# Performance work log

Measured on AMD Instinct MI355X. Metric: run time of the kernel, lower is better.

The kernel has to match this reference:

```python
import jax, jax.numpy as jnp
import numpy as np

M_CACHE, N_MODEL, D_HEAD = 8192, 4096, 128
H_HEADS = N_MODEL // D_HEAD  # 32
SEQ_LEN = 16


def setup_inputs() -> dict:
    key = jax.random.key(0)
    ks = jax.random.split(key, 6)
    X = jax.random.normal(ks[0], (SEQ_LEN, N_MODEL), dtype=jnp.float32)
    W_q = jax.random.normal(ks[1], (N_MODEL, N_MODEL), dtype=jnp.float32) * 0.02
    W_k = jax.random.normal(ks[2], (N_MODEL, N_MODEL), dtype=jnp.float32) * 0.02
    W_v = jax.random.normal(ks[3], (N_MODEL, N_MODEL), dtype=jnp.float32) * 0.02
    cache_K = jax.random.normal(ks[4], (H_HEADS, M_CACHE, D_HEAD), dtype=jnp.float32)
    cache_V = jax.random.normal(ks[5], (H_HEADS, M_CACHE, D_HEAD), dtype=jnp.float32)
    return {"X": X, "W_q": W_q, "W_k": W_k, "W_v": W_v,
            "cache_K": cache_K, "cache_V": cache_V, "P": 4096}


def reference(X, W_q, W_k, W_v, cache_K, cache_V, P):
    S = X.shape[0]
    H, M, D = cache_K.shape
    # QKV projections, split into heads: [S, N] -> [H, S, D]
    q = (X @ W_q).reshape(S, H, D).transpose(1, 0, 2)
    k = (X @ W_k).reshape(S, H, D).transpose(1, 0, 2)
    v = (X @ W_v).reshape(S, H, D).transpose(1, 0, 2)
    # KV-cache slice write at position P
    cK = cache_K.at[:, P:P + S, :].set(k)
    cV = cache_V.at[:, P:P + S, :].set(v)
    # Unscaled attention over the FULL cache length (faithful to original)
    scores = jnp.einsum('hsd,hmd->hsm', q, cK)          # [H, S, M]
    weights = jax.nn.softmax(scores, axis=-1)
    out = jnp.einsum('hsm,hmd->hsd', weights, cV)        # [H, S, D]
    # Original does .view(S, H*D) on the [H, S, D] tensor (no transpose)
    return out.reshape(S, H * D)
```

## Files before the change

kernel.cpp:

```cpp
#include <hip/hip_runtime.h>

#define S_LEN 16
#define NMODEL 4096
#define DHEAD 128
#define HHEADS 32
#define MCACHE 8192
#define SPLITK 32
#define KSLICE (NMODEL / SPLITK)
#define CHUNK_W 32
#define NCHT (MCACHE / CHUNK_W)
#define MPAD 36

#define PART_ELEMS   ((size_t)3 * SPLITK * S_LEN * NMODEL)
#define OPART_USH    ((size_t)HHEADS * NCHT * S_LEN * DHEAD)
#define OPART_FLOATS (OPART_USH / 2)
#define REGION_ELEMS (PART_ELEMS > OPART_FLOATS ? PART_ELEMS : OPART_FLOATS)
#define STAT_ELEMS   ((size_t)HHEADS * NCHT * S_LEN)

typedef _Float16 half8 __attribute__((ext_vector_type(8)));
typedef float    f32x4 __attribute__((ext_vector_type(4)));

__device__ __forceinline__ half8 cvt8(float4 a, float4 b) {
    half8 h;
    h[0] = (_Float16)a.x; h[1] = (_Float16)a.y; h[2] = (_Float16)a.z; h[3] = (_Float16)a.w;
    h[4] = (_Float16)b.x; h[5] = (_Float16)b.y; h[6] = (_Float16)b.z; h[7] = (_Float16)b.w;
    return h;
}
__device__ __forceinline__ unsigned short f2h(float f) {
    _Float16 h = (_Float16)f; unsigned short u; __builtin_memcpy(&u, &h, 2); return u;
}
__device__ __forceinline__ float h2f(unsigned short u) {
    _Float16 h; __builtin_memcpy(&h, &u, 2); return (float)h;
}

__global__ __launch_bounds__(256) void qkv_gemm(const float* __restrict__ X,
                                                const float* __restrict__ Wq,
                                                const float* __restrict__ Wk,
                                                const float* __restrict__ Wv,
                                                float* __restrict__ part) {
    const int tid   = threadIdx.x;
    const int col2  = blockIdx.x * 256 + tid;
    const int split = blockIdx.y;
    const int mat   = blockIdx.z;
    const float* __restrict__ W = (mat == 0) ? Wq : (mat == 1) ? Wk : Wv;
    const int k0 = split * KSLICE;

    __shared__ float Xs[KSLICE][S_LEN];
    for (int i = tid; i < KSLICE * S_LEN; i += 256) {
        const int s = i & 15, k = i >> 4;
        Xs[k][s] = X[s * NMODEL + k0 + k];
    }
    __syncthreads();

    float2 acc[S_LEN];
#pragma unroll
    for (int s = 0; s < S_LEN; ++s) { acc[s].x = 0.f; acc[s].y = 0.f; }

    const float2* __restrict__ Wp = (const float2*)(W + (size_t)k0 * NMODEL) + col2;

#pragma unroll 8
    for (int k = 0; k < KSLICE; ++k) {
        const float2 w = Wp[(size_t)k * (NMODEL / 2)];
        const float4* __restrict__ xr = (const float4*)&Xs[k][0];
#pragma unroll
        for (int s4 = 0; s4 < 4; ++s4) {
            const float4 xv = xr[s4];
            acc[s4 * 4 + 0].x += xv.x * w.x;  acc[s4 * 4 + 0].y += xv.x * w.y;
            acc[s4 * 4 + 1].x += xv.y * w.x;  acc[s4 * 4 + 1].y += xv.y * w.y;
            acc[s4 * 4 + 2].x += xv.z * w.x;  acc[s4 * 4 + 2].y += xv.z * w.y;
            acc[s4 * 4 + 3].x += xv.w * w.x;  acc[s4 * 4 + 3].y += xv.w * w.y;
        }
    }

    float2* __restrict__ pp =
        (float2*)(part + (size_t)(mat * SPLITK + split) * S_LEN * NMODEL) + col2;
#pragma unroll
    for (int s = 0; s < S_LEN; ++s) pp[(size_t)s * (NMODEL / 2)] = acc[s];
}

__global__ __launch_bounds__(256) void qkv_reduce(const float* __restrict__ part,
                                                  float* __restrict__ qkv) {
    const int i4   = blockIdx.x * 256 + threadIdx.x;
    const int flat = i4 * 4;
    const int mat  = flat / (S_LEN * NMODEL);
    const int rem  = flat % (S_LEN * NMODEL);
    float4 sum = {0.f, 0.f, 0.f, 0.f};
#pragma unroll 8
    for (int sp = 0; sp < SPLITK; ++sp) {
        const float4 v = *(const float4*)(part +
            (size_t)(mat * SPLITK + sp) * (S_LEN * NMODEL) + rem);
        sum.x += v.x; sum.y += v.y; sum.z += v.z; sum.w += v.w;
    }
    *(float4*)(qkv + flat) = sum;
}

__global__ __launch_bounds__(128) void attn_partial(const float* __restrict__ qkv,
                                                    const float* __restrict__ cacheK,
                                                    const float* __restrict__ cacheV,
                                                    const int* __restrict__ Pp,
                                                    unsigned short* __restrict__ opart,
                                                    float* __restrict__ mstat,
                                                    float* __restrict__ lstat) {
    const int bx   = blockIdx.x;
    const int h    = blockIdx.y;
    const int tid  = threadIdx.x;
    const int wv   = tid >> 6;
    const int lane = tid & 63;
    const int c    = bx * 2 + wv;
    const int c0   = c * CHUNK_W;
    const int P    = *Pp;
    const int lo   = (P > c0) ? P : c0;
    const int hi_  = (P + S_LEN < c0 + CHUNK_W) ? (P + S_LEN) : (c0 + CHUNK_W);
    const bool overlap = (lo < hi_);

    const float* qb = qkv;
    const float* kb = qkv + S_LEN * NMODEL;
    const float* vb = qkv + 2 * S_LEN * NMODEL;

    __shared__ float scs[2][S_LEN][MPAD];
    __shared__ float ml[2][S_LEN], ll[2][S_LEN];

    const int row16 = lane & 15;
    const int kg    = lane >> 4;

    {
        half8 qf[4];
#pragma unroll
        for (int cs = 0; cs < 4; ++cs) {
            const float* qr = qb + row16 * NMODEL + h * DHEAD + cs * 32 + kg * 8;
            qf[cs] = cvt8(*(const float4*)qr, *(const float4*)(qr + 4));
        }
#pragma unroll
        for (int t = 0; t < 2; ++t) {
            const float* krow = cacheK +
                ((size_t)h * MCACHE + c0 + t * 16 + row16) * DHEAD + kg * 8;
            f32x4 acc = {0.f, 0.f, 0.f, 0.f};
#pragma unroll
            for (int cs = 0; cs < 4; ++cs) {
                const float4 ka = *(const float4*)(krow + cs * 32);
                const float4 kc = *(const float4*)(krow + cs * 32 + 4);
                acc = __builtin_amdgcn_mfma_f32_16x16x32_f16(qf[cs], cvt8(ka, kc),
                                                             acc, 0, 0, 0);
            }
#pragma unroll
            for (int r = 0; r < 4; ++r)
                scs[wv][kg * 4 + r][t * 16 + row16] = acc[r];
        }

        if (overlap) {
            const int sq = kg, dsl = row16, doff = dsl * 8;
            float4 q0[4], q1[4];
#pragma unroll
            for (int j = 0; j < 4; ++j) {
                const int s = sq * 4 + j;
                q0[j] = *(const float4*)(qb + s * NMODEL + h * DHEAD + doff);
                q1[j] = *(const float4*)(qb + s * NMODEL + h * DHEAD + doff + 4);
            }
            for (int gm = lo; gm < hi_; ++gm) {
                const float* kr = kb + (size_t)(gm - P) * NMODEL + h * DHEAD + doff;
                const float4 ka = *(const float4*)(kr);
                const float4 kc = *(const float4*)(kr + 4);
                float pr[4];
#pragma unroll
                for (int j = 0; j < 4; ++j) {
                    pr[j] = ka.x * q0[j].x + ka.y * q0[j].y + ka.z * q0[j].z + ka.w * q0[j].w
                          + kc.x * q1[j].x + kc.y * q1[j].y + kc.z * q1[j].z + kc.w * q1[j].w;
                }
#pragma unroll
                for (int j = 0; j < 4; ++j) {
                    float v = pr[j];
                    v += __shfl_xor(v, 1, 64);
                    v += __shfl_xor(v, 2, 64);
                    v += __shfl_xor(v, 4, 64);
                    v += __shfl_xor(v, 8, 64);
                    pr[j] = v;
                }
                if (dsl == 0) {
#pragma unroll
                    for (int j = 0; j < 4; ++j)
                        scs[wv][sq * 4 + j][gm - c0] = pr[j];
                }
            }
        }
    }
    __syncthreads();

    {
        const int rl = lane & 31;
        for (int s = 0; s < S_LEN; ++s) {
            const float v = scs[wv][s][rl];
            float mx = v;
            for (int off = 16; off > 0; off >>= 1) mx = fmaxf(mx, __shfl_xor(mx, off, 64));
            const float e = __expf(v - mx);
            scs[wv][s][rl] = e;
            float sum = e;
            for (int off = 16; off > 0; off >>= 1) sum += __shfl_xor(sum, off, 64);
            if (lane == 0) { ml[wv][s] = mx; ll[wv][s] = sum; }
        }
    }
    __syncthreads();

    {
        const int sq = lane >> 4, dsl = lane & 15, doff = dsl * 8;
        const float* vbase = cacheV + ((size_t)h * MCACHE + c0) * DHEAD + doff;
        float a[4][8];
#pragma unroll
        for (int j = 0; j < 4; ++j)
#pragma unroll
            for (int k = 0; k < 8; ++k) a[j][k] = 0.f;

        for (int m = 0; m < CHUNK_W; ++m) {
            const float4 v0 = *(const float4*)(vbase + (size_t)m * DHEAD);
            const float4 v1 = *(const float4*)(vbase + (size_t)m * DHEAD + 4);
            const float pj0 = scs[wv][sq * 4 + 0][m];
            const float pj1 = scs[wv][sq * 4 + 1][m];
            const float pj2 = scs[wv][sq * 4 + 2][m];
            const float pj3 = scs[wv][sq * 4 + 3][m];
            const float pj[4] = {pj0, pj1, pj2, pj3};
#pragma unroll
            for (int j = 0; j < 4; ++j) {
                a[j][0] += pj[j] * v0.x; a[j][1] += pj[j] * v0.y;
                a[j][2] += pj[j] * v0.z; a[j][3] += pj[j] * v0.w;
                a[j][4] += pj[j] * v1.x; a[j][5] += pj[j] * v1.y;
                a[j][6] += pj[j] * v1.z; a[j][7] += pj[j] * v1.w;
            }
        }

        if (overlap) {
            for (int gm = lo; gm < hi_; ++gm) {
                const float* vn = vb + (size_t)(gm - P) * NMODEL + h * DHEAD + doff;
                const float* vo = cacheV + ((size_t)h * MCACHE + gm) * DHEAD + doff;
                const float4 n0 = *(const float4*)(vn);
                const float4 n1 = *(const float4*)(vn + 4);
                const float4 o0 = *(const float4*)(vo);
                const float4 o1 = *(const float4*)(vo + 4);
                const int i = gm - c0;
                const float pj[4] = {scs[wv][sq * 4 + 0][i], scs[wv][sq * 4 + 1][i],
                                     scs[wv][sq * 4 + 2][i], scs[wv][sq * 4 + 3][i]};
#pragma unroll
                for (int j = 0; j < 4; ++j) {
                    a[j][0] += pj[j] * (n0.x - o0.x); a[j][1] += pj[j] * (n0.y - o0.y);
                    a[j][2] += pj[j] * (n0.z - o0.z); a[j][3] += pj[j] * (n0.w - o0.w);
                    a[j][4] += pj[j] * (n1.x - o1.x); a[j][5] += pj[j] * (n1.y - o1.y);
                    a[j][6] += pj[j] * (n1.z - o1.z); a[j][7] += pj[j] * (n1.w - o1.w);
                }
            }
        }

        const size_t ob = ((size_t)h * NCHT + c) * S_LEN * DHEAD;
#pragma unroll
        for (int j = 0; j < 4; ++j) {
            const int s = sq * 4 + j;
            uint4 pk;
            unsigned short* us = (unsigned short*)&pk;
#pragma unroll
            for (int k = 0; k < 8; ++k) us[k] = f2h(a[j][k]);
            *(uint4*)&opart[ob + (size_t)s * DHEAD + doff] = pk;
        }
    }

    if (tid < 32) {
        const int w2 = tid >> 4, s = tid & 15;
        const int cc = bx * 2 + w2;
        mstat[((size_t)h * S_LEN + s) * NCHT + cc] = ml[w2][s];
        lstat[((size_t)h * S_LEN + s) * NCHT + cc] = ll[w2][s];
    }
}

__global__ __launch_bounds__(512) void attn_combine(const unsigned short* __restrict__ opart,
                                                    const float* __restrict__ mstat,
                                                    const float* __restrict__ lstat,
                                                    float* __restrict__ out) {
    const int tid = threadIdx.x;
    const int cg  = tid >> 7;
    const int d   = tid & 127;
    const int s   = blockIdx.x;
    const int h   = blockIdx.y;

    __shared__ float mlds[NCHT], llds[NCHT], wlds[NCHT];
    __shared__ float olds[4][DHEAD];
    __shared__ float Llds[4];

    const size_t sb = ((size_t)h * S_LEN + s) * NCHT;
    if (tid < NCHT) { mlds[tid] = mstat[sb + tid]; llds[tid] = lstat[sb + tid]; }
    __syncthreads();

    float gmax = fmaxf(fmaxf(mlds[tid & 63], mlds[(tid & 63) + 64]),
                       fmaxf(mlds[(tid & 63) + 128], mlds[(tid & 63) + 192]));
    for (int off = 32; off > 0; off >>= 1) gmax = fmaxf(gmax, __shfl_xor(gmax, off, 64));

    if (tid < NCHT) wlds[tid] = __expf(mlds[tid] - gmax);
    __syncthreads();

    float o = 0.f, L = 0.f;
    for (int c = cg; c < NCHT; c += 4) {
        const float w = wlds[c];
        o += w * h2f(opart[(((size_t)h * NCHT + c) * S_LEN + s) * DHEAD + d]);
        L += w * llds[c];
    }
    olds[cg][d] = o;
    if (d == 0) Llds[cg] = L;
    __syncthreads();

    if (tid < DHEAD) {
        const float ot = olds[0][tid] + olds[1][tid] + olds[2][tid] + olds[3][tid];
        const float Lt = Llds[0] + Llds[1] + Llds[2] + Llds[3];
        out[((size_t)h * S_LEN + s) * DHEAD + tid] = ot / Lt;
    }
}

extern "C" void kernel_launch(void* const* d_in, const int* in_sizes, int n_in,
                              void* d_out, int out_size, void* d_ws, size_t ws_size,
                              hipStream_t stream) {
    const float* X      = (const float*)d_in[0];
    const float* Wq     = (const float*)d_in[1];
    const float* Wk     = (const float*)d_in[2];
    const float* Wv     = (const float*)d_in[3];
    const float* cacheK = (const float*)d_in[4];
    const float* cacheV = (const float*)d_in[5];
    const int*   P      = (const int*)d_in[6];
    float* out = (float*)d_out;
    float* ws  = (float*)d_ws;

    float*          qkv   = ws;
    float*          part  = qkv + 3 * S_LEN * NMODEL;
    unsigned short* opart = (unsigned short*)part;
    float*          mstat = part + REGION_ELEMS;
    float*          lstat = mstat + STAT_ELEMS;

    qkv_gemm<<<dim3(8, SPLITK, 3), 256, 0, stream>>>(X, Wq, Wk, Wv, part);
    qkv_reduce<<<(3 * S_LEN * NMODEL / 4) / 256, 256, 0, stream>>>(part, qkv);
    attn_partial<<<dim3(NCHT / 2, HHEADS), 128, 0, stream>>>(qkv, cacheK, cacheV, P,
                                                             opart, mstat, lstat);
    attn_combine<<<dim3(S_LEN, HHEADS), 512, 0, stream>>>(opart, mstat, lstat, out);
}
```

Baseline: 163.6 us.

## Double attention chunk width and vectorize softmax and combine loads

Doubles the per-wave cache chunk from 32 to 64 positions, which halves the number of partial outputs and stats written to workspace and then reduced in the combine kernel. The per-chunk softmax is restructured so each lane handles 16 contiguous scores of one query row with float4 LDS access and a 2-step shuffle, instead of 16 serial row loops. The combine kernel reads packed half pairs and uses 8 chunk groups. The cost is more per-wave work and a larger LDS score buffer, which may lower parallelism and occupancy in the main attention kernel.

```diff
diff --git a/kernel.cpp b/kernel.cpp
--- a/kernel.cpp
+++ b/kernel.cpp
@@ -7,9 +7,9 @@
 #define MCACHE 8192
 #define SPLITK 32
 #define KSLICE (NMODEL / SPLITK)
-#define CHUNK_W 32
+#define CHUNK_W 64
 #define NCHT (MCACHE / CHUNK_W)
-#define MPAD 36
+#define MPAD 68
 
 #define PART_ELEMS   ((size_t)3 * SPLITK * S_LEN * NMODEL)
 #define OPART_USH    ((size_t)HHEADS * NCHT * S_LEN * DHEAD)
@@ -131,7 +131,7 @@
             qf[cs] = cvt8(*(const float4*)qr, *(const float4*)(qr + 4));
         }
 #pragma unroll
-        for (int t = 0; t < 2; ++t) {
+        for (int t = 0; t < 4; ++t) {
             const float* krow = cacheK +
                 ((size_t)h * MCACHE + c0 + t * 16 + row16) * DHEAD + kg * 8;
             f32x4 acc = {0.f, 0.f, 0.f, 0.f};
@@ -186,17 +186,40 @@
     __syncthreads();
 
     {
-        const int rl = lane & 31;
-        for (int s = 0; s < S_LEN; ++s) {
-            const float v = scs[wv][s][rl];
-            float mx = v;
-            for (int off = 16; off > 0; off >>= 1) mx = fmaxf(mx, __shfl_xor(mx, off, 64));
-            const float e = __expf(v - mx);
-            scs[wv][s][rl] = e;
-            float sum = e;
-            for (int off = 16; off > 0; off >>= 1) sum += __shfl_xor(sum, off, 64);
-            if (lane == 0) { ml[wv][s] = mx; ll[wv][s] = sum; }
-        }
+        const int s  = lane >> 2;
+        const int mg = lane & 3;
+        float4 v0 = *(const float4*)&scs[wv][s][mg * 16];
+        float4 v1 = *(const float4*)&scs[wv][s][mg * 16 + 4];
+        float4 v2 = *(const float4*)&scs[wv][s][mg * 16 + 8];
+        float4 v3 = *(const float4*)&scs[wv][s][mg * 16 + 12];
+
+        float mx = fmaxf(fmaxf(fmaxf(v0.x, v0.y), fmaxf(v0.z, v0.w)),
+                         fmaxf(fmaxf(v1.x, v1.y), fmaxf(v1.z, v1.w)));
+        mx = fmaxf(mx, fmaxf(fmaxf(fmaxf(v2.x, v2.y), fmaxf(v2.z, v2.w)),
+                             fmaxf(fmaxf(v3.x, v3.y), fmaxf(v3.z, v3.w))));
+        mx = fmaxf(mx, __shfl_xor(mx, 1, 64));
+        mx = fmaxf(mx, __shfl_xor(mx, 2, 64));
+
+        v0.x = __expf(v0.x - mx); v0.y = __expf(v0.y - mx);
+        v0.z = __expf(v0.z - mx); v0.w = __expf(v0.w - mx);
+        v1.x = __expf(v1.x - mx); v1.y = __expf(v1.y - mx);
+        v1.z = __expf(v1.z - mx); v1.w = __expf(v1.w - mx);
+        v2.x = __expf(v2.x - mx); v2.y = __expf(v2.y - mx);
+        v2.z = __expf(v2.z - mx); v2.w = __expf(v2.w - mx);
+        v3.x = __expf(v3.x - mx); v3.y = __expf(v3.y - mx);
+        v3.z = __expf(v3.z - mx); v3.w = __expf(v3.w - mx);
+
+        float sum = (v0.x + v0.y + v0.z + v0.w) + (v1.x + v1.y + v1.z + v1.w)
+                  + (v2.x + v2.y + v2.z + v2.w) + (v3.x + v3.y + v3.z + v3.w);
+        sum += __shfl_xor(sum, 1, 64);
+        sum += __shfl_xor(sum, 2, 64);
+
+        *(float4*)&scs[wv][s][mg * 16]      = v0;
+        *(float4*)&scs[wv][s][mg * 16 + 4]  = v1;
+        *(float4*)&scs[wv][s][mg * 16 + 8]  = v2;
+        *(float4*)&scs[wv][s][mg * 16 + 12] = v3;
+
+        if (mg == 0) { ml[wv][s] = mx; ll[wv][s] = sum; }
     }
     __syncthreads();
 
@@ -210,13 +233,10 @@
             for (int k = 0; k < 8; ++k) a[j][k] = 0.f;
 
         for (int m = 0; m < CHUNK_W; ++m) {
+            const float pj[4] = {scs[wv][sq * 4 + 0][m], scs[wv][sq * 4 + 1][m],
+                                 scs[wv][sq * 4 + 2][m], scs[wv][sq * 4 + 3][m]};
             const float4 v0 = *(const float4*)(vbase + (size_t)m * DHEAD);
             const float4 v1 = *(const float4*)(vbase + (size_t)m * DHEAD + 4);
-            const float pj0 = scs[wv][sq * 4 + 0][m];
-            const float pj1 = scs[wv][sq * 4 + 1][m];
-            const float pj2 = scs[wv][sq * 4 + 2][m];
-            const float pj3 = scs[wv][sq * 4 + 3][m];
-            const float pj[4] = {pj0, pj1, pj2, pj3};
 #pragma unroll
             for (int j = 0; j < 4; ++j) {
                 a[j][0] += pj[j] * v0.x; a[j][1] += pj[j] * v0.y;
@@ -228,15 +248,15 @@
 
         if (overlap) {
             for (int gm = lo; gm < hi_; ++gm) {
+                const int i = gm - c0;
+                const float pj[4] = {scs[wv][sq * 4 + 0][i], scs[wv][sq * 4 + 1][i],
+                                     scs[wv][sq * 4 + 2][i], scs[wv][sq * 4 + 3][i]};
                 const float* vn = vb + (size_t)(gm - P) * NMODEL + h * DHEAD + doff;
                 const float* vo = cacheV + ((size_t)h * MCACHE + gm) * DHEAD + doff;
                 const float4 n0 = *(const float4*)(vn);
                 const float4 n1 = *(const float4*)(vn + 4);
                 const float4 o0 = *(const float4*)(vo);
                 const float4 o1 = *(const float4*)(vo + 4);
-                const int i = gm - c0;
-                const float pj[4] = {scs[wv][sq * 4 + 0][i], scs[wv][sq * 4 + 1][i],
-                                     scs[wv][sq * 4 + 2][i], scs[wv][sq * 4 + 3][i]};
 #pragma unroll
                 for (int j = 0; j < 4; ++j) {
                     a[j][0] += pj[j] * (n0.x - o0.x); a[j][1] += pj[j] * (n0.y - o0.y);
@@ -272,39 +292,43 @@
                                                     const float* __restrict__ lstat,
                                                     float* __restrict__ out) {
     const int tid = threadIdx.x;
-    const int cg  = tid >> 7;
-    const int d   = tid & 127;
+    const int dp  = tid & 63;
+    const int cg  = tid >> 6;
     const int s   = blockIdx.x;
     const int h   = blockIdx.y;
 
     __shared__ float mlds[NCHT], llds[NCHT], wlds[NCHT];
-    __shared__ float olds[4][DHEAD];
-    __shared__ float Llds[4];
+    __shared__ float olds[8][DHEAD];
+    __shared__ float Llds[8];
 
     const size_t sb = ((size_t)h * S_LEN + s) * NCHT;
     if (tid < NCHT) { mlds[tid] = mstat[sb + tid]; llds[tid] = lstat[sb + tid]; }
     __syncthreads();
 
-    float gmax = fmaxf(fmaxf(mlds[tid & 63], mlds[(tid & 63) + 64]),
-                       fmaxf(mlds[(tid & 63) + 128], mlds[(tid & 63) + 192]));
+    float gmax = fmaxf(mlds[tid & 63], mlds[(tid & 63) + 64]);
     for (int off = 32; off > 0; off >>= 1) gmax = fmaxf(gmax, __shfl_xor(gmax, off, 64));
 
     if (tid < NCHT) wlds[tid] = __expf(mlds[tid] - gmax);
     __syncthreads();
 
-    float o = 0.f, L = 0.f;
-    for (int c = cg; c < NCHT; c += 4) {
+    float ox = 0.f, oy = 0.f, L = 0.f;
+    for (int c = cg; c < NCHT; c += 8) {
         const float w = wlds[c];
-        o += w * h2f(opart[(((size_t)h * NCHT + c) * S_LEN + s) * DHEAD + d]);
-        L += w * llds[c];
-    }
-    olds[cg][d] = o;
-    if (d == 0) Llds[cg] = L;
+        const unsigned int u = *(const unsigned int*)
+            &opart[(((size_t)h * NCHT + c) * S_LEN + s) * DHEAD + dp * 2];
+        ox += w * h2f((unsigned short)(u & 0xffffu));
+        oy += w * h2f((unsigned short)(u >> 16));
+        L  += w * llds[c];
+    }
+    olds[cg][dp * 2]     = ox;
+    olds[cg][dp * 2 + 1] = oy;
+    if (dp == 0) Llds[cg] = L;
     __syncthreads();
 
     if (tid < DHEAD) {
-        const float ot = olds[0][tid] + olds[1][tid] + olds[2][tid] + olds[3][tid];
-        const float Lt = Llds[0] + Llds[1] + Llds[2] + Llds[3];
+        float ot = 0.f, Lt = 0.f;
+#pragma unroll
+        for (int g = 0; g < 8; ++g) { ot += olds[g][tid]; Lt += Llds[g]; }
         out[((size_t)h * S_LEN + s) * DHEAD + tid] = ot / Lt;
     }
 }
```

Result: faster. 140.2 us (-14.3%).
